# Kernel optimization log

Measured on AMD Instinct MI355X. Metric: run time of the kernel, lower is better.

## Reference

```python
import jax, jax.numpy as jnp
import numpy as np

DIM = 1024
GRID_SIZE = 5
SPLINE_ORDER = 3
N_TOKENS = 8192
EPS = 1e-6


def setup_inputs() -> dict:
    key = jax.random.key(0)
    k1, k2, k3 = jax.random.split(key, 3)
    x = jax.random.normal(k1, (N_TOKENS, DIM), dtype=jnp.float32)
    norm_weight = jnp.ones((DIM,), dtype=jnp.float32)
    # nn.Linear default init ~ U(-1/sqrt(dim), 1/sqrt(dim)); randn scaled is fine for a numeric baseline
    base_weight = jax.random.normal(k2, (DIM, DIM), dtype=jnp.float32) * (1.0 / np.sqrt(DIM))
    spline_weight = jax.random.normal(k3, (DIM, GRID_SIZE), dtype=jnp.float32) * 0.1
    gamma = jnp.full((DIM,), 1e-5, dtype=jnp.float32)
    return {"x": x, "norm_weight": norm_weight, "base_weight": base_weight,
            "spline_weight": spline_weight, "gamma": gamma}


def _knots():
    h = 2.0 / GRID_SIZE
    n_knots = GRID_SIZE + SPLINE_ORDER + 1
    return jnp.linspace(-1.0 - SPLINE_ORDER * h, 1.0 + SPLINE_ORDER * h, n_knots)


def _b_spline_basis(x_clamped, knots):
    # x_clamped: (N, D) -> bases: (N, D, grid_size)
    xe = x_clamped[..., None]  # (N, D, 1)
    bases = ((xe >= knots[:-1]) & (xe < knots[1:])).astype(x_clamped.dtype)
    for k in range(1, SPLINE_ORDER + 1):  # fixed small unroll (Cox-de Boor)
        n = bases.shape[-1] - 1
        left_den = jnp.maximum(knots[k:k + n] - knots[:n], 1e-8)
        left = (xe - knots[:n]) / left_den * bases[..., :n]
        right_den = jnp.maximum(knots[k + 1:k + 1 + n] - knots[1:1 + n], 1e-8)
        right = (knots[k + 1:k + 1 + n] - xe) / right_den * bases[..., 1:1 + n]
        bases = left + right
    return bases


def reference(x, norm_weight, base_weight, spline_weight, gamma):
    knots = _knots()
    # RMSNorm
    xf = x.astype(jnp.float32)
    x_norm = (xf * jax.lax.rsqrt(jnp.mean(xf * xf, axis=-1, keepdims=True) + EPS)).astype(x.dtype)
    x_norm = x_norm * norm_weight
    # base path: Linear(dim, dim, bias=False) -> x @ W.T
    base_out = x_norm @ base_weight.T
    # spline path
    x_clamped = jnp.clip(x_norm, -1.0, 1.0)
    spline_bases = _b_spline_basis(x_clamped, knots)  # (N, D, grid_size)
    spline_out = jnp.einsum('ndb,db->nd', spline_bases, spline_weight)
    return x + (base_out + spline_out) * gamma
```

## Files before the change

### kernel.cpp

```cpp
#include <hip/hip_runtime.h>
#include <hip/hip_bf16.h>
#include <stdint.h>

#define DIM 1024
#define NTOK 8192

#define BM 128
#define BN 128
#define BK 64

typedef unsigned char uchar;
typedef __attribute__((ext_vector_type(4)))  int   i32x4;
typedef __attribute__((ext_vector_type(8)))  int   i32x8;
typedef __attribute__((ext_vector_type(4)))  float f32x4;
typedef __attribute__((ext_vector_type(16))) float f32x16;

#define GLOAD_LDS16(g, l)                                                \
    __builtin_amdgcn_global_load_lds(                                    \
        (const __attribute__((address_space(1))) void*)(g),              \
        (__attribute__((address_space(3))) void*)(l), 16, 0, 0)

__device__ __forceinline__ unsigned short f2bf(float f) {
    union { float f; uint32_t u; } v; v.f = f;
    uint32_t u = v.u;
    u += 0x7FFFu + ((u >> 16) & 1u);
    return (unsigned short)(u >> 16);
}
__device__ __forceinline__ float bf2f(unsigned short h) {
    union { uint32_t u; float f; } v; v.u = ((uint32_t)h) << 16; return v.f;
}

__device__ __forceinline__ float spline_eval(float xn, float s0, float s1,
                                             float s2, float s3, float s4) {
    const float xc = fminf(fmaxf(xn, -1.0f), 1.0f);
    const float u = (xc + 2.2f) * (1.0f / 0.55f);
    int j = (int)u;
    j = j < 2 ? 2 : (j > 5 ? 5 : j);
    const float t = u - (float)j;
    const float omt = 1.0f - t;
    const float t2 = t * t, t3 = t2 * t;
    const float w0 = omt * omt * omt * (1.0f / 6.0f);
    const float w1 = (3.0f * t3 - 6.0f * t2 + 4.0f) * (1.0f / 6.0f);
    const float w2 = (-3.0f * t3 + 3.0f * t2 + 3.0f * t + 1.0f) * (1.0f / 6.0f);
    const float w3 = t3 * (1.0f / 6.0f);
    float so;
    if (j == 2)      so = w1 * s0 + w2 * s1 + w3 * s2;
    else if (j == 3) so = w0 * s0 + w1 * s1 + w2 * s2 + w3 * s3;
    else if (j == 4) so = w0 * s1 + w1 * s2 + w2 * s3 + w3 * s4;
    else             so = w0 * s2 + w1 * s3 + w2 * s4;
    return so;
}

__device__ __forceinline__ int pack_fp8x4(float a, float b, float c, float d) {
    int p = __builtin_amdgcn_cvt_pk_fp8_f32(a, b, 0, false);
    p = __builtin_amdgcn_cvt_pk_fp8_f32(c, d, p, true);
    return p;
}

__global__ __launch_bounds__(256) void prep_kernel(
    const float* __restrict__ x, const float* __restrict__ nw,
    const float* __restrict__ W,
    uchar* __restrict__ xn8, uchar* __restrict__ W8,
    float* __restrict__ rr)
{
    const int bid = blockIdx.x;
    const int t = threadIdx.x;
    const int lane = t & 63, w = t >> 6;

    if (bid >= NTOK / 4) {
        const int row = (bid - NTOK / 4) * 4 + w;
        const float4* src = reinterpret_cast<const float4*>(W + (size_t)row * DIM) + lane * 4;
        const float4 a = src[0], b = src[1], c = src[2], d = src[3];
        int4 o;
        o.x = pack_fp8x4(a.x, a.y, a.z, a.w);
        o.y = pack_fp8x4(b.x, b.y, b.z, b.w);
        o.z = pack_fp8x4(c.x, c.y, c.z, c.w);
        o.w = pack_fp8x4(d.x, d.y, d.z, d.w);
        reinterpret_cast<int4*>(W8 + (size_t)row * DIM)[lane] = o;
        return;
    }

    const int row = bid * 4 + w;
    const float4* xr = reinterpret_cast<const float4*>(x + (size_t)row * DIM) + lane * 4;
    const float4 a = xr[0], b = xr[1], c = xr[2], d = xr[3];

    float ssq = a.x*a.x + a.y*a.y + a.z*a.z + a.w*a.w
              + b.x*b.x + b.y*b.y + b.z*b.z + b.w*b.w
              + c.x*c.x + c.y*c.y + c.z*c.z + c.w*c.w
              + d.x*d.x + d.y*d.y + d.z*d.z + d.w*d.w;
    #pragma unroll
    for (int off = 32; off; off >>= 1) ssq += __shfl_xor(ssq, off, 64);

    const float r = rsqrtf(ssq * (1.0f / DIM) + 1e-6f);
    if (lane == 0) rr[row] = r;

    const float4* nwr = reinterpret_cast<const float4*>(nw) + lane * 4;
    const float4 na = nwr[0], nb = nwr[1], nc = nwr[2], nd = nwr[3];
    int4 o;
    o.x = pack_fp8x4(a.x*r*na.x, a.y*r*na.y, a.z*r*na.z, a.w*r*na.w);
    o.y = pack_fp8x4(b.x*r*nb.x, b.y*r*nb.y, b.z*r*nb.z, b.w*r*nb.w);
    o.z = pack_fp8x4(c.x*r*nc.x, c.y*r*nc.y, c.z*r*nc.z, c.w*r*nc.w);
    o.w = pack_fp8x4(d.x*r*nd.x, d.y*r*nd.y, d.z*r*nd.z, d.w*r*nd.w);
    reinterpret_cast<int4*>(xn8 + (size_t)row * DIM)[lane] = o;
}

__global__ __launch_bounds__(256, 2) void gemm_ep_kernel(
    const uchar* __restrict__ A,
    const uchar* __restrict__ B,
    const float* __restrict__ x,
    const float* __restrict__ rrow,
    const float* __restrict__ nw,
    const float* __restrict__ sw,
    const float* __restrict__ gamma,
    float* __restrict__ out)
{
    __shared__ uchar SB[4 * 16384];

    const int tid = threadIdx.x;
    const int lane = tid & 63, wid = tid >> 6;

    const int bid = blockIdx.x;
    const int swz = (bid & 7) * 64 + (bid >> 3);
    const int bm = swz >> 3, bn = swz & 7;

    const int wm = wid >> 1, wn = wid & 1;

    f32x16 acc[2][2] = {};

    const int srow = tid >> 2;
    const int scol = ((tid & 3) ^ ((tid >> 3) & 3)) * 16;
    const uchar* Ag = A + (size_t)(bm * BM + srow) * DIM + scol;
    const uchar* Bg = B + (size_t)(bn * BN + srow) * DIM + scol;
    const int oA = tid * 16;
    const int oB = 8192 + tid * 16;

    const int xorv = (lane >> 1) & 3;
    const int u0 = ((lane >> 5) * 2) ^ xorv;
    const int u1 = u0 ^ 1;
    const int aBase = (wm * 64 + (lane & 31)) * 64;
    const int bBase = 8192 + (wn * 64 + (lane & 31)) * 64;

#define STAGE(bi, kt) do {                                           \
        uchar* sb_ = SB + (bi) * 16384;                              \
        const uchar* a_ = Ag + (size_t)(kt) * BK;                    \
        const uchar* b_ = Bg + (size_t)(kt) * BK;                    \
        GLOAD_LDS16(a_,            sb_ + oA);                        \
        GLOAD_LDS16(a_ + 64 * DIM, sb_ + oA + 4096);                 \
        GLOAD_LDS16(b_,            sb_ + oB);                        \
        GLOAD_LDS16(b_ + 64 * DIM, sb_ + oB + 4096);                 \
    } while (0)

#define LD8(dst, base) do {                                          \
        const i32x4 lo_ = *reinterpret_cast<const i32x4*>(sb_ + (base) + u0 * 16); \
        const i32x4 hi_ = *reinterpret_cast<const i32x4*>(sb_ + (base) + u1 * 16); \
        dst = (i32x8){lo_[0], lo_[1], lo_[2], lo_[3],                \
                      hi_[0], hi_[1], hi_[2], hi_[3]};               \
    } while (0)

#define COMP(bi) do {                                                \
        const uchar* sb_ = SB + (bi) * 16384;                        \
        i32x8 a0, a1, b0, b1;                                        \
        LD8(a0, aBase);                                              \
        LD8(a1, aBase + 2048);                                       \
        LD8(b0, bBase);                                              \
        LD8(b1, bBase + 2048);                                       \
        acc[0][0] = __builtin_amdgcn_mfma_scale_f32_32x32x64_f8f6f4( \
            a0, b0, acc[0][0], 0, 0, 0, 0x7F7F7F7F, 0, 0x7F7F7F7F);  \
        acc[0][1] = __builtin_amdgcn_mfma_scale_f32_32x32x64_f8f6f4( \
            a0, b1, acc[0][1], 0, 0, 0, 0x7F7F7F7F, 0, 0x7F7F7F7F);  \
        acc[1][0] = __builtin_amdgcn_mfma_scale_f32_32x32x64_f8f6f4( \
            a1, b0, acc[1][0], 0, 0, 0, 0x7F7F7F7F, 0, 0x7F7F7F7F);  \
        acc[1][1] = __builtin_amdgcn_mfma_scale_f32_32x32x64_f8f6f4( \
            a1, b1, acc[1][1], 0, 0, 0, 0x7F7F7F7F, 0, 0x7F7F7F7F);  \
    } while (0)

#define W8v asm volatile("s_waitcnt vmcnt(8)" ::: "memory")
#define W4v asm volatile("s_waitcnt vmcnt(4)" ::: "memory")
#define W0v asm volatile("s_waitcnt vmcnt(0)" ::: "memory")
#define BAR __builtin_amdgcn_s_barrier()

    STAGE(0, 0);
    STAGE(1, 1);
    #pragma unroll 1
    for (int k4 = 0; k4 < 12; k4 += 4) {
        STAGE(2, k4 + 2); W8v; BAR; COMP(0);
        STAGE(3, k4 + 3); W8v; BAR; COMP(1);
        STAGE(0, k4 + 4); W8v; BAR; COMP(2);
        STAGE(1, k4 + 5); W8v; BAR; COMP(3);
    }
    STAGE(2, 14); W8v; BAR; COMP(0);
    STAGE(3, 15); W8v; BAR; COMP(1);
    W4v; BAR; COMP(2);
    W0v; BAR; COMP(3);
    __syncthreads();

#undef STAGE
#undef LD8
#undef COMP
#undef W8v
#undef W4v
#undef W0v
#undef BAR

    unsigned short* Cb = reinterpret_cast<unsigned short*>(SB);
    {
        const int crow0 = wm * 64 + 4 * (lane >> 5);
        const int ccol0 = wn * 64 + (lane & 31);
        #pragma unroll
        for (int i = 0; i < 2; ++i)
            #pragma unroll
            for (int j = 0; j < 2; ++j)
                #pragma unroll
                for (int r = 0; r < 16; ++r) {
                    const int lr = crow0 + i * 32 + (r & 3) + 8 * (r >> 2);
                    Cb[lr * 136 + ccol0 + j * 32] = f2bf(acc[i][j][r]);
                }
    }
    __syncthreads();

    const int colg = bn * BN + (tid & 31) * 4;
    float sf[20];
    {
        const float4* swp = reinterpret_cast<const float4*>(sw + (size_t)colg * 5);
        #pragma unroll
        for (int q = 0; q < 5; ++q) {
            const float4 w4 = swp[q];
            sf[q * 4 + 0] = w4.x; sf[q * 4 + 1] = w4.y;
            sf[q * 4 + 2] = w4.z; sf[q * 4 + 3] = w4.w;
        }
    }
    const float4 gv  = *reinterpret_cast<const float4*>(gamma + colg);
    const float4 nwv = *reinterpret_cast<const float4*>(nw + colg);

    #pragma unroll
    for (int v = 0; v < 16; ++v) {
        const int lr = (tid >> 5) * 16 + v;
        const size_t grow = (size_t)(bm * BM + lr);
        const ushort4 cb4 = *reinterpret_cast<const ushort4*>(&Cb[lr * 136 + (tid & 31) * 4]);
        const float4 xv = *reinterpret_cast<const float4*>(x + grow * DIM + colg);
        const float rv = rrow[grow];
        float4 ov;
        ov.x = xv.x + (bf2f(cb4.x) + spline_eval(xv.x * rv * nwv.x, sf[0],  sf[1],  sf[2],  sf[3],  sf[4]))  * gv.x;
        ov.y = xv.y + (bf2f(cb4.y) + spline_eval(xv.y * rv * nwv.y, sf[5],  sf[6],  sf[7],  sf[8],  sf[9]))  * gv.y;
        ov.z = xv.z + (bf2f(cb4.z) + spline_eval(xv.z * rv * nwv.z, sf[10], sf[11], sf[12], sf[13], sf[14])) * gv.z;
        ov.w = xv.w + (bf2f(cb4.w) + spline_eval(xv.w * rv * nwv.w, sf[15], sf[16], sf[17], sf[18], sf[19])) * gv.w;
        *reinterpret_cast<float4*>(out + grow * DIM + colg) = ov;
    }
}

extern "C" void kernel_launch(void* const* d_in, const int* in_sizes, int n_in,
                              void* d_out, int out_size, void* d_ws, size_t ws_size,
                              hipStream_t stream) {
    const float* x     = (const float*)d_in[0];
    const float* nw    = (const float*)d_in[1];
    const float* W     = (const float*)d_in[2];
    const float* sw    = (const float*)d_in[3];
    const float* gamma = (const float*)d_in[4];
    float* out = (float*)d_out;

    uchar* xn8 = (uchar*)d_ws;
    uchar* W8  = xn8 + (size_t)NTOK * DIM;
    float* rr  = (float*)(W8 + (size_t)DIM * DIM);

    prep_kernel<<<dim3(NTOK / 4 + DIM / 4), 256, 0, stream>>>(x, nw, W, xn8, W8, rr);
    gemm_ep_kernel<<<dim3((NTOK / BM) * (DIM / BN)), 256, 0, stream>>>(
        xn8, W8, x, rr, nw, sw, gamma, out);
}
```

Measured before the change: 41.83 us.

## Halve GEMM M-tile to 64 rows and raise occupancy to three blocks per CU

Shrinks the block tile from 128x128 to 64x128, so each wave computes two MFMA tiles instead of four. LDS per stage drops to 12 KB, and launch bounds now allow three blocks per CU. The wait counts and block-index swizzle are adjusted to match. The intent is more blocks in flight (1024 instead of 512) to balance across CUs and hide latency, at the cost of reloading the B tile twice as often and lower MFMA-to-load reuse.

```diff
diff --git a/kernel.cpp b/kernel.cpp
--- a/kernel.cpp
+++ b/kernel.cpp
@@ -5,7 +5,7 @@
 #define DIM 1024
 #define NTOK 8192
 
-#define BM 128
+#define BM 64
 #define BN 128
 #define BK 64
 
@@ -104,7 +104,7 @@
     reinterpret_cast<int4*>(xn8 + (size_t)row * DIM)[lane] = o;
 }
 
-__global__ __launch_bounds__(256, 2) void gemm_ep_kernel(
+__global__ __launch_bounds__(256, 3) void gemm_ep_kernel(
     const uchar* __restrict__ A,
     const uchar* __restrict__ B,
     const float* __restrict__ x,
@@ -114,38 +114,38 @@
     const float* __restrict__ gamma,
     float* __restrict__ out)
 {
-    __shared__ uchar SB[4 * 16384];
+    __shared__ uchar SB[4 * 12288];
 
     const int tid = threadIdx.x;
     const int lane = tid & 63, wid = tid >> 6;
 
     const int bid = blockIdx.x;
-    const int swz = (bid & 7) * 64 + (bid >> 3);
-    const int bm = swz >> 3, bn = swz & 7;
+    const int local = bid >> 3;
+    const int bn = local & 7;
+    const int bm = (bid & 7) * 16 + (local >> 3);
 
     const int wm = wid >> 1, wn = wid & 1;
 
-    f32x16 acc[2][2] = {};
+    f32x16 acc[2] = {};
 
     const int srow = tid >> 2;
     const int scol = ((tid & 3) ^ ((tid >> 3) & 3)) * 16;
     const uchar* Ag = A + (size_t)(bm * BM + srow) * DIM + scol;
     const uchar* Bg = B + (size_t)(bn * BN + srow) * DIM + scol;
     const int oA = tid * 16;
-    const int oB = 8192 + tid * 16;
+    const int oB = 4096 + tid * 16;
 
     const int xorv = (lane >> 1) & 3;
     const int u0 = ((lane >> 5) * 2) ^ xorv;
     const int u1 = u0 ^ 1;
-    const int aBase = (wm * 64 + (lane & 31)) * 64;
-    const int bBase = 8192 + (wn * 64 + (lane & 31)) * 64;
+    const int aBase = (wm * 32 + (lane & 31)) * 64;
+    const int bBase = 4096 + (wn * 64 + (lane & 31)) * 64;
 
 #define STAGE(bi, kt) do {                                           \
-        uchar* sb_ = SB + (bi) * 16384;                              \
+        uchar* sb_ = SB + (bi) * 12288;                              \
         const uchar* a_ = Ag + (size_t)(kt) * BK;                    \
         const uchar* b_ = Bg + (size_t)(kt) * BK;                    \
         GLOAD_LDS16(a_,            sb_ + oA);                        \
-        GLOAD_LDS16(a_ + 64 * DIM, sb_ + oA + 4096);                 \
         GLOAD_LDS16(b_,            sb_ + oB);                        \
         GLOAD_LDS16(b_ + 64 * DIM, sb_ + oB + 4096);                 \
     } while (0)
@@ -158,24 +158,19 @@
     } while (0)
 
 #define COMP(bi) do {                                                \
-        const uchar* sb_ = SB + (bi) * 16384;                        \
-        i32x8 a0, a1, b0, b1;                                        \
+        const uchar* sb_ = SB + (bi) * 12288;                        \
+        i32x8 a0, b0, b1;                                            \
         LD8(a0, aBase);                                              \
-        LD8(a1, aBase + 2048);                                       \
         LD8(b0, bBase);                                              \
         LD8(b1, bBase + 2048);                                       \
-        acc[0][0] = __builtin_amdgcn_mfma_scale_f32_32x32x64_f8f6f4( \
-            a0, b0, acc[0][0], 0, 0, 0, 0x7F7F7F7F, 0, 0x7F7F7F7F);  \
-        acc[0][1] = __builtin_amdgcn_mfma_scale_f32_32x32x64_f8f6f4( \
-            a0, b1, acc[0][1], 0, 0, 0, 0x7F7F7F7F, 0, 0x7F7F7F7F);  \
-        acc[1][0] = __builtin_amdgcn_mfma_scale_f32_32x32x64_f8f6f4( \
-            a1, b0, acc[1][0], 0, 0, 0, 0x7F7F7F7F, 0, 0x7F7F7F7F);  \
-        acc[1][1] = __builtin_amdgcn_mfma_scale_f32_32x32x64_f8f6f4( \
-            a1, b1, acc[1][1], 0, 0, 0, 0x7F7F7F7F, 0, 0x7F7F7F7F);  \
+        acc[0] = __builtin_amdgcn_mfma_scale_f32_32x32x64_f8f6f4(    \
+            a0, b0, acc[0], 0, 0, 0, 0x7F7F7F7F, 0, 0x7F7F7F7F);     \
+        acc[1] = __builtin_amdgcn_mfma_scale_f32_32x32x64_f8f6f4(    \
+            a0, b1, acc[1], 0, 0, 0, 0x7F7F7F7F, 0, 0x7F7F7F7F);     \
     } while (0)
 
-#define W8v asm volatile("s_waitcnt vmcnt(8)" ::: "memory")
-#define W4v asm volatile("s_waitcnt vmcnt(4)" ::: "memory")
+#define W6v asm volatile("s_waitcnt vmcnt(6)" ::: "memory")
+#define W3v asm volatile("s_waitcnt vmcnt(3)" ::: "memory")
 #define W0v asm volatile("s_waitcnt vmcnt(0)" ::: "memory")
 #define BAR __builtin_amdgcn_s_barrier()
 
@@ -183,38 +178,36 @@
     STAGE(1, 1);
     #pragma unroll 1
     for (int k4 = 0; k4 < 12; k4 += 4) {
-        STAGE(2, k4 + 2); W8v; BAR; COMP(0);
-        STAGE(3, k4 + 3); W8v; BAR; COMP(1);
-        STAGE(0, k4 + 4); W8v; BAR; COMP(2);
-        STAGE(1, k4 + 5); W8v; BAR; COMP(3);
-    }
-    STAGE(2, 14); W8v; BAR; COMP(0);
-    STAGE(3, 15); W8v; BAR; COMP(1);
-    W4v; BAR; COMP(2);
+        STAGE(2, k4 + 2); W6v; BAR; COMP(0);
+        STAGE(3, k4 + 3); W6v; BAR; COMP(1);
+        STAGE(0, k4 + 4); W6v; BAR; COMP(2);
+        STAGE(1, k4 + 5); W6v; BAR; COMP(3);
+    }
+    STAGE(2, 14); W6v; BAR; COMP(0);
+    STAGE(3, 15); W6v; BAR; COMP(1);
+    W3v; BAR; COMP(2);
     W0v; BAR; COMP(3);
     __syncthreads();
 
 #undef STAGE
 #undef LD8
 #undef COMP
-#undef W8v
-#undef W4v
+#undef W6v
+#undef W3v
 #undef W0v
 #undef BAR
 
     unsigned short* Cb = reinterpret_cast<unsigned short*>(SB);
     {
-        const int crow0 = wm * 64 + 4 * (lane >> 5);
+        const int crow0 = wm * 32 + 4 * (lane >> 5);
         const int ccol0 = wn * 64 + (lane & 31);
         #pragma unroll
-        for (int i = 0; i < 2; ++i)
+        for (int j = 0; j < 2; ++j)
             #pragma unroll
-            for (int j = 0; j < 2; ++j)
-                #pragma unroll
-                for (int r = 0; r < 16; ++r) {
-                    const int lr = crow0 + i * 32 + (r & 3) + 8 * (r >> 2);
-                    Cb[lr * 136 + ccol0 + j * 32] = f2bf(acc[i][j][r]);
-                }
+            for (int r = 0; r < 16; ++r) {
+                const int lr = crow0 + (r & 3) + 8 * (r >> 2);
+                Cb[lr * 136 + ccol0 + j * 32] = f2bf(acc[j][r]);
+            }
     }
     __syncthreads();
 
@@ -233,8 +226,8 @@
     const float4 nwv = *reinterpret_cast<const float4*>(nw + colg);
 
     #pragma unroll
-    for (int v = 0; v < 16; ++v) {
-        const int lr = (tid >> 5) * 16 + v;
+    for (int v = 0; v < 8; ++v) {
+        const int lr = (tid >> 5) * 8 + v;
         const size_t grow = (size_t)(bm * BM + lr);
         const ushort4 cb4 = *reinterpret_cast<const ushort4*>(&Cb[lr * 136 + (tid & 31) * 4]);
         const float4 xv = *reinterpret_cast<const float4*>(x + grow * DIM + colg);
```

New measurement: 42.94 us. 1.03x slower.
